# Kernel optimization log

Measured on AMD Instinct MI355X. Metric: run time of the kernel, lower is better.

The kernel has to match this reference:

```python
import jax, jax.numpy as jnp
import numpy as np

D = 1024
H = 16
HD = D // H
MAX_LEN = 5000
LN_EPS = 1e-5


def _pos_encoding(seq_len, d_model, dtype=jnp.float32):
    pos = jnp.arange(seq_len, dtype=jnp.float32)[:, None]                      # [S,1]
    div = jnp.exp(jnp.arange(0, d_model, 2, dtype=jnp.float32) * (-np.log(10000.0) / d_model))
    pe = jnp.zeros((seq_len, d_model), dtype=jnp.float32)
    pe = pe.at[:, 0::2].set(jnp.sin(pos * div))
    pe = pe.at[:, 1::2].set(jnp.cos(pos * div))
    return pe.astype(dtype)                                                    # [S,D]


def _layer_norm(x, g, b):
    mu = jnp.mean(x, axis=-1, keepdims=True)
    var = jnp.mean(jnp.square(x - mu), axis=-1, keepdims=True)
    return (x - mu) * jax.lax.rsqrt(var + LN_EPS) * g + b


def setup_inputs() -> dict:
    key = jax.random.key(0)
    ks = jax.random.split(key, 12)
    B, S = 2, 2048
    s = 1.0 / np.sqrt(D)
    return {
        "key": jax.random.normal(ks[0], (B, S, D), jnp.float32),
        "value": jax.random.normal(ks[1], (B, S, D), jnp.float32),
        "query": jax.random.normal(ks[2], (B, S, D), jnp.float32),
        "Wq": jax.random.normal(ks[3], (D, D), jnp.float32) * s,
        "Wk": jax.random.normal(ks[4], (D, D), jnp.float32) * s,
        "Wv": jax.random.normal(ks[5], (D, D), jnp.float32) * s,
        "Wo": jax.random.normal(ks[6], (D, D), jnp.float32) * s,
        "W1": jax.random.normal(ks[7], (D, D), jnp.float32) * s,
        "b1": jnp.zeros((D,), jnp.float32),
        "W2": jax.random.normal(ks[8], (D, D), jnp.float32) * s,
        "b2": jnp.zeros((D,), jnp.float32),
        "ln1_g": jnp.ones((D,), jnp.float32),
        "ln1_b": jnp.zeros((D,), jnp.float32),
        "ln2_g": jnp.ones((D,), jnp.float32),
        "ln2_b": jnp.zeros((D,), jnp.float32),
    }


def reference(key, value, query, Wq, Wk, Wv, Wo, W1, b1, W2, b2, ln1_g, ln1_b, ln2_g, ln2_b):
    B, S, _ = query.shape
    pe = _pos_encoding(S, D, query.dtype)                 # [S,D]
    k = key + pe
    v = value + pe
    q = query + pe
    # QKV projections (torch Linear: x @ W.T), split heads -> [B,H,S,HD]
    qh = (q @ Wq.T).reshape(B, S, H, HD).transpose(0, 2, 1, 3)
    kh = (k @ Wk.T).reshape(B, S, H, HD).transpose(0, 2, 1, 3)
    vh = (v @ Wv.T).reshape(B, S, H, HD).transpose(0, 2, 1, 3)
    # scaled dot-product attention (full score matrix, as in source)
    scores = jnp.einsum('bhqd,bhkd->bhqk', qh, kh) / np.sqrt(HD)
    attn = jax.nn.softmax(scores, axis=-1)
    ctx = jnp.einsum('bhqk,bhkd->bhqd', attn, vh)         # [B,H,S,HD]
    ctx = ctx.transpose(0, 2, 1, 3).reshape(B, S, D)
    attn_out = ctx @ Wo.T
    # add & norm (residual = pos-encoded query)
    x = _layer_norm(attn_out + q, ln1_g, ln1_b)
    # position-wise FFN (hidden == input_dim)
    ff = jax.nn.relu(x @ W1.T + b1) @ W2.T + b2
    return _layer_norm(ff + x, ln2_g, ln2_b)
```

## Files before the change

kernel.cpp:

```cpp
#include <hip/hip_runtime.h>
#include <hip/hip_bf16.h>
#include <math.h>


#define B_ 2
#define S_ 2048
#define D_ 1024
#define H_ 16
#define HD_ 64

typedef __bf16 bf16_t;
typedef __bf16 bf16x8 __attribute__((ext_vector_type(8)));
typedef __bf16 bf16x4v __attribute__((ext_vector_type(4)));
typedef float f32x4 __attribute__((ext_vector_type(4)));
typedef float f32x16 __attribute__((ext_vector_type(16)));
typedef unsigned int u32;

__device__ __forceinline__ f32x4 mfma16(bf16x8 a, bf16x8 b, f32x4 c) {
  return __builtin_amdgcn_mfma_f32_16x16x32_bf16(a, b, c, 0, 0, 0);
}
__device__ __forceinline__ f32x16 mfma32(bf16x8 a, bf16x8 b, f32x16 c) {
  return __builtin_amdgcn_mfma_f32_32x32x16_bf16(a, b, c, 0, 0, 0);
}
__device__ __forceinline__ u32 pkbf(float a, float b) {
  union { bf16_t h[2]; u32 u; } t;
  t.h[0] = (bf16_t)a; t.h[1] = (bf16_t)b;
  return t.u;
}

__device__ __forceinline__ void gload_lds16(const bf16_t* g, bf16_t* l) {
  __builtin_amdgcn_global_load_lds((const __attribute__((address_space(1))) void*)g,
                                   (__attribute__((address_space(3))) void*)l,
                                   16, 0, 0);
}

__global__ __launch_bounds__(256) void cvtw_kernel(
    const float* __restrict__ w0, const float* __restrict__ w1,
    const float* __restrict__ w2, const float* __restrict__ w3,
    const float* __restrict__ w4, const float* __restrict__ w5,
    bf16_t* __restrict__ dst) {
  const int wsel = blockIdx.y;
  const float* src = wsel == 0 ? w0 : wsel == 1 ? w1 : wsel == 2 ? w2
                   : wsel == 3 ? w3 : wsel == 4 ? w4 : w5;
  const size_t off = (size_t)blockIdx.x * 1024 + threadIdx.x * 4;
  float4 v = *(const float4*)(src + off);
  bf16x4v r;
  r[0] = (bf16_t)v.x; r[1] = (bf16_t)v.y; r[2] = (bf16_t)v.z; r[3] = (bf16_t)v.w;
  *(bf16x4v*)(dst + (size_t)wsel * (D_ * D_) + off) = r;
}

__global__ __launch_bounds__(256) void addpe_kernel(
    const float* __restrict__ q, const float* __restrict__ k,
    const float* __restrict__ v,
    bf16_t* __restrict__ qo, bf16_t* __restrict__ ko, bf16_t* __restrict__ vo) {
  const int row = blockIdx.x;
  const int s = row & (S_ - 1);
  const int d0 = threadIdx.x * 4;
  const size_t base = (size_t)row * D_ + d0;
  float pe[4];
#pragma unroll
  for (int p = 0; p < 2; ++p) {
    float div = __expf((float)(d0 + 2 * p) * -0.008994473019508f);
    float ang = (float)s * div;
    pe[2 * p]     = sinf(ang);
    pe[2 * p + 1] = cosf(ang);
  }
  float4 qv = *(const float4*)&q[base];
  float4 kv = *(const float4*)&k[base];
  float4 vv = *(const float4*)&v[base];
  bf16x4v qr, kr, vr;
  qr[0] = (bf16_t)(qv.x + pe[0]); qr[1] = (bf16_t)(qv.y + pe[1]);
  qr[2] = (bf16_t)(qv.z + pe[2]); qr[3] = (bf16_t)(qv.w + pe[3]);
  kr[0] = (bf16_t)(kv.x + pe[0]); kr[1] = (bf16_t)(kv.y + pe[1]);
  kr[2] = (bf16_t)(kv.z + pe[2]); kr[3] = (bf16_t)(kv.w + pe[3]);
  vr[0] = (bf16_t)(vv.x + pe[0]); vr[1] = (bf16_t)(vv.y + pe[1]);
  vr[2] = (bf16_t)(vv.z + pe[2]); vr[3] = (bf16_t)(vv.w + pe[3]);
  *(bf16x4v*)&qo[base] = qr;
  *(bf16x4v*)&ko[base] = kr;
  *(bf16x4v*)&vo[base] = vr;
}

template <int EPI>
__global__ __launch_bounds__(256) void gemm_s(
    const bf16_t* __restrict__ A, const bf16_t* __restrict__ Wb,
    const float* __restrict__ bias, bf16_t* __restrict__ C) {
  constexpr int Kd = 1024, NT = Kd / 32;
  __shared__ alignas(16) bf16_t As[2][128 * 32];
  __shared__ alignas(16) bf16_t Bs[2][64 * 32];
  const int t = threadIdx.x, lane = t & 63, wid = t >> 6;
  const int m0 = blockIdx.y * 128, n0 = blockIdx.x * 64;

  const bf16_t* Asrc0 = A + (size_t)(m0 + wid * 16 + (lane >> 2)) * Kd + (lane & 3) * 8;
  const bf16_t* Asrc1 = Asrc0 + (size_t)64 * Kd;
  const bf16_t* Wsrc = Wb + (size_t)(n0 + wid * 16 + (lane >> 2)) * Kd + (lane & 3) * 8;

  const f32x4 zero = {0.f, 0.f, 0.f, 0.f};
  f32x4 acc[4][2];
#pragma unroll
  for (int m = 0; m < 4; ++m) { acc[m][0] = zero; acc[m][1] = zero; }

  gload_lds16(Asrc0, &As[0][wid * 512]);
  gload_lds16(Asrc1, &As[0][2048 + wid * 512]);
  gload_lds16(Wsrc,  &Bs[0][wid * 512]);

  const int wr = wid >> 1, wc = wid & 1;
#pragma unroll 2
  for (int kt = 0; kt < NT; ++kt) {
    __syncthreads();
    const int cur = kt & 1, nxt = cur ^ 1;
    if (kt + 1 < NT) {
      const int k0 = (kt + 1) * 32;
      gload_lds16(Asrc0 + k0, &As[nxt][wid * 512]);
      gload_lds16(Asrc1 + k0, &As[nxt][2048 + wid * 512]);
      gload_lds16(Wsrc + k0,  &Bs[nxt][wid * 512]);
    }
    bf16x8 af[4], bfr[2];
#pragma unroll
    for (int m = 0; m < 4; ++m)
      af[m] = *(const bf16x8*)&As[cur][(wr * 64 + m * 16 + (lane & 15)) * 32 + (lane >> 4) * 8];
#pragma unroll
    for (int n = 0; n < 2; ++n)
      bfr[n] = *(const bf16x8*)&Bs[cur][(wc * 32 + n * 16 + (lane & 15)) * 32 + (lane >> 4) * 8];
    __builtin_amdgcn_s_setprio(1);
#pragma unroll
    for (int m = 0; m < 4; ++m)
#pragma unroll
      for (int n = 0; n < 2; ++n)
        acc[m][n] = mfma16(af[m], bfr[n], acc[m][n]);
    __builtin_amdgcn_s_setprio(0);
  }

  const int rbase = m0 + wr * 64 + (lane >> 4) * 4;
  const int cbase = n0 + wc * 32 + (lane & 15);
#pragma unroll
  for (int n = 0; n < 2; ++n) {
    const int col = cbase + n * 16;
    float bv = (EPI >= 1) ? bias[col] : 0.f;
#pragma unroll
    for (int m = 0; m < 4; ++m)
#pragma unroll
      for (int r = 0; r < 4; ++r) {
        float vv = acc[m][n][r] + bv;
        if (EPI == 2) vv = fmaxf(vv, 0.f);
        C[(size_t)(rbase + m * 16 + r) * D_ + col] = (bf16_t)vv;
      }
  }
}

__global__ __launch_bounds__(256) void gemm_qkv(
    const bf16_t* __restrict__ a0p, const bf16_t* __restrict__ a1p,
    const bf16_t* __restrict__ a2p,
    const bf16_t* __restrict__ w0p, const bf16_t* __restrict__ w1p,
    const bf16_t* __restrict__ w2p,
    bf16_t* __restrict__ o0, bf16_t* __restrict__ o1, bf16_t* __restrict__ o2) {
  constexpr int Kd = 1024, NT = Kd / 32;
  __shared__ alignas(16) bf16_t As[2][128 * 32];
  __shared__ alignas(16) bf16_t Bs[2][128 * 32];
  const int t = threadIdx.x, lane = t & 63, wid = t >> 6;
  const int g = lane >> 4, c16 = lane & 15;
  const int m0 = blockIdx.y * 128, n0 = blockIdx.x * 128;

  const bf16_t* A = a0p;
  const bf16_t* Wb = w0p;
  if (blockIdx.z == 1) { A = a1p; Wb = w1p; }
  else if (blockIdx.z == 2) { A = a2p; Wb = w2p; }

  const bf16_t* Asrc0 = A + (size_t)(m0 + wid * 16 + (lane >> 2)) * Kd + (lane & 3) * 8;
  const bf16_t* Asrc1 = Asrc0 + (size_t)64 * Kd;
  const bf16_t* Wsrc0 = Wb + (size_t)(n0 + wid * 16 + (lane >> 2)) * Kd + (lane & 3) * 8;
  const bf16_t* Wsrc1 = Wsrc0 + (size_t)64 * Kd;

  const f32x4 zero = {0.f, 0.f, 0.f, 0.f};
  f32x4 acc[4][4];
#pragma unroll
  for (int m = 0; m < 4; ++m)
#pragma unroll
    for (int n = 0; n < 4; ++n) acc[m][n] = zero;

  gload_lds16(Asrc0, &As[0][wid * 512]);
  gload_lds16(Asrc1, &As[0][2048 + wid * 512]);
  gload_lds16(Wsrc0, &Bs[0][wid * 512]);
  gload_lds16(Wsrc1, &Bs[0][2048 + wid * 512]);

  const int wr = wid >> 1, wc = wid & 1;
#pragma unroll 2
  for (int kt = 0; kt < NT; ++kt) {
    __syncthreads();
    const int cur = kt & 1, nxt = cur ^ 1;
    if (kt + 1 < NT) {
      const int k0 = (kt + 1) * 32;
      gload_lds16(Asrc0 + k0, &As[nxt][wid * 512]);
      gload_lds16(Asrc1 + k0, &As[nxt][2048 + wid * 512]);
      gload_lds16(Wsrc0 + k0, &Bs[nxt][wid * 512]);
      gload_lds16(Wsrc1 + k0, &Bs[nxt][2048 + wid * 512]);
    }
    bf16x8 af[4], bfr[4];
#pragma unroll
    for (int m = 0; m < 4; ++m)
      af[m] = *(const bf16x8*)&As[cur][(wr * 64 + m * 16 + c16) * 32 + g * 8];
#pragma unroll
    for (int n = 0; n < 4; ++n)
      bfr[n] = *(const bf16x8*)&Bs[cur][(wc * 64 + n * 16 + c16) * 32 + g * 8];
    __builtin_amdgcn_s_setprio(1);
#pragma unroll
    for (int m = 0; m < 4; ++m)
#pragma unroll
      for (int n = 0; n < 4; ++n)
        acc[m][n] = mfma16(af[m], bfr[n], acc[m][n]);
    __builtin_amdgcn_s_setprio(0);
  }

  const int rbase = m0 + wr * 64 + g * 4;
  const int cbase = n0 + wc * 64 + c16;
  if (blockIdx.z == 2) {
#pragma unroll
    for (int n = 0; n < 4; ++n) {
      const int col = cbase + n * 16;
#pragma unroll
      for (int m = 0; m < 4; ++m)
#pragma unroll
        for (int r = 0; r < 4; ++r) {
          const int row = rbase + m * 16 + r;
          const int bb = row >> 11, ss = row & (S_ - 1);
          o2[(size_t)bb * D_ * S_ + (size_t)col * S_ + ss] = (bf16_t)acc[m][n][r];
        }
    }
  } else {
    bf16_t* C = (blockIdx.z == 1) ? o1 : o0;
#pragma unroll
    for (int n = 0; n < 4; ++n) {
      const int col = cbase + n * 16;
#pragma unroll
      for (int m = 0; m < 4; ++m)
#pragma unroll
        for (int r = 0; r < 4; ++r)
          C[(size_t)(rbase + m * 16 + r) * D_ + col] = (bf16_t)acc[m][n][r];
    }
  }
}

__global__ __launch_bounds__(256) void attn_kernel(
    const bf16_t* __restrict__ Q, const bf16_t* __restrict__ K,
    const bf16_t* __restrict__ Vt, bf16_t* __restrict__ O) {
  constexpr int NT = S_ / 64;
  constexpr float THR = 11.5416f;
  __shared__ alignas(16) bf16_t Ks[2][64 * 64];
  __shared__ alignas(16) bf16_t Vs[2][64 * 64];
  const int t = threadIdx.x, lane = t & 63, wid = t >> 6;
  const int b = blockIdx.y >> 4, h = blockIdx.y & 15;
  const int qw = blockIdx.x * 128 + wid * 32;
  const int q31 = lane & 31, hi = lane >> 5;

  bf16x8 qb[4];
  {
    const size_t qrow = (size_t)(b * S_ + qw + q31) * D_ + h * HD_ + hi * 8;
#pragma unroll
    for (int ksl = 0; ksl < 4; ++ksl) {
      bf16x8 v = *(const bf16x8*)&Q[qrow + ksl * 16];
#pragma unroll
      for (int j = 0; j < 8; ++j)
        v[j] = (bf16_t)((float)v[j] * (0.125f * 1.44269504f));
      qb[ksl] = v;
    }
  }
  bf16x8 onesb;
#pragma unroll
  for (int j = 0; j < 8; ++j) onesb[j] = (bf16_t)1.0f;

  f32x16 ctx0 = {0.f,0.f,0.f,0.f,0.f,0.f,0.f,0.f,0.f,0.f,0.f,0.f,0.f,0.f,0.f,0.f};
  f32x16 ctx1 = ctx0, lf = ctx0;
  float mrow = -1e30f;

  int sw[4];
#pragma unroll
  for (int x = 0; x < 4; ++x) sw[x] = ((x * 2 + hi) ^ (q31 & 7)) * 8;

  const int trow = wid * 8 + (lane >> 3);
  const int krow_g = (trow & ~12) | ((trow & 4) << 1) | ((trow & 8) >> 1);
  const int lslot = ((lane & 7) ^ ((lane >> 3) & 7)) * 8;
  const bf16_t* Ksrc0 = K + (size_t)(b * S_ + krow_g) * D_ + h * HD_ + lslot;
  const bf16_t* Ksrc1 = K + (size_t)(b * S_ + 32 + krow_g) * D_ + h * HD_ + lslot;
  const bf16_t* Vsrc0 = Vt + (size_t)b * D_ * S_ + (size_t)(h * HD_ + trow) * S_ + lslot;
  const bf16_t* Vsrc1 = Vt + (size_t)b * D_ * S_ + (size_t)(h * HD_ + 32 + trow) * S_ + lslot;

  gload_lds16(Ksrc0, &Ks[0][wid * 512]);
  gload_lds16(Ksrc1, &Ks[0][2048 + wid * 512]);
  gload_lds16(Vsrc0, &Vs[0][wid * 512]);
  gload_lds16(Vsrc1, &Vs[0][2048 + wid * 512]);

#pragma unroll 2
  for (int kt = 0; kt < NT; ++kt) {
    __syncthreads();
    const int cur = kt & 1, nxt = cur ^ 1;
    if (kt + 1 < NT) {
      const size_t ko = (size_t)(kt + 1) * 64 * D_;
      gload_lds16(Ksrc0 + ko, &Ks[nxt][wid * 512]);
      gload_lds16(Ksrc1 + ko, &Ks[nxt][2048 + wid * 512]);
      const size_t vo = (size_t)(kt + 1) * 64;
      gload_lds16(Vsrc0 + vo, &Vs[nxt][wid * 512]);
      gload_lds16(Vsrc1 + vo, &Vs[nxt][2048 + wid * 512]);
    }

    f32x16 s0 = {0.f,0.f,0.f,0.f,0.f,0.f,0.f,0.f,0.f,0.f,0.f,0.f,0.f,0.f,0.f,0.f};
    f32x16 s1 = s0;
    __builtin_amdgcn_s_setprio(1);
#pragma unroll
    for (int ksl = 0; ksl < 4; ++ksl) {
      bf16x8 kb0 = *(const bf16x8*)&Ks[cur][q31 * 64 + sw[ksl]];
      bf16x8 kb1 = *(const bf16x8*)&Ks[cur][(32 + q31) * 64 + sw[ksl]];
      s0 = mfma32(kb0, qb[ksl], s0);
      s1 = mfma32(kb1, qb[ksl], s1);
    }
    __builtin_amdgcn_s_setprio(0);

    float mt = fmaxf(s0[0], s1[0]);
#pragma unroll
    for (int r = 1; r < 16; ++r) mt = fmaxf(mt, fmaxf(s0[r], s1[r]));
    mt = fmaxf(mt, __shfl_xor(mt, 32));
    if (__any(mt > mrow + THR)) {
      float mnew = fmaxf(mrow, mt);
      float scl = exp2f(mrow - mnew);
      mrow = mnew;
#pragma unroll
      for (int r = 0; r < 16; ++r) {
        float sc = __shfl(scl, (r & 3) + 8 * (r >> 2) + 4 * hi);
        ctx0[r] *= sc; ctx1[r] *= sc; lf[r] *= sc;
      }
    }
#pragma unroll
    for (int r = 0; r < 16; ++r) {
      s0[r] = exp2f(s0[r] - mrow);
      s1[r] = exp2f(s1[r] - mrow);
    }

    bf16x8 pa[4];
#pragma unroll
    for (int ks = 0; ks < 4; ++ks) {
      union { u32 w[4]; bf16x8 v; } u;
      if (ks < 2) {
#pragma unroll
        for (int w = 0; w < 4; ++w)
          u.w[w] = pkbf(s0[(ks & 1) * 8 + 2 * w], s0[(ks & 1) * 8 + 2 * w + 1]);
      } else {
#pragma unroll
        for (int w = 0; w < 4; ++w)
          u.w[w] = pkbf(s1[(ks & 1) * 8 + 2 * w], s1[(ks & 1) * 8 + 2 * w + 1]);
      }
      pa[ks] = u.v;
    }

    __builtin_amdgcn_s_setprio(1);
#pragma unroll
    for (int ks = 0; ks < 4; ++ks) lf = mfma32(pa[ks], onesb, lf);
#pragma unroll
    for (int ks = 0; ks < 4; ++ks) {
      bf16x8 vb0 = *(const bf16x8*)&Vs[cur][q31 * 64 + sw[ks]];
      bf16x8 vb1 = *(const bf16x8*)&Vs[cur][(32 + q31) * 64 + sw[ks]];
      ctx0 = mfma32(pa[ks], vb0, ctx0);
      ctx1 = mfma32(pa[ks], vb1, ctx1);
    }
    __builtin_amdgcn_s_setprio(0);
  }

#pragma unroll
  for (int r = 0; r < 16; ++r) {
    const int q = (r & 3) + 8 * (r >> 2) + 4 * hi;
    const float inv = 1.f / lf[r];
    const size_t ro = (size_t)(b * S_ + qw + q) * D_ + h * HD_ + q31;
    O[ro]      = (bf16_t)(ctx0[r] * inv);
    O[ro + 32] = (bf16_t)(ctx1[r] * inv);
  }
}

template <typename OUT>
__global__ __launch_bounds__(256) void add_ln_kernel(
    const bf16_t* __restrict__ a, const bf16_t* __restrict__ res,
    const float* __restrict__ g, const float* __restrict__ be,
    OUT* __restrict__ out) {
  const int t = threadIdx.x;
  const int d0 = t * 4;
  const size_t base = (size_t)blockIdx.x * D_ + d0;
  bf16x4v av = *(const bf16x4v*)&a[base];
  bf16x4v rv = *(const bf16x4v*)&res[base];
  float x[4];
  float s1 = 0.f, s2 = 0.f;
#pragma unroll
  for (int e = 0; e < 4; ++e) {
    x[e] = (float)av[e] + (float)rv[e];
    s1 += x[e];
    s2 += x[e] * x[e];
  }
#pragma unroll
  for (int o = 32; o > 0; o >>= 1) {
    s1 += __shfl_down(s1, o);
    s2 += __shfl_down(s2, o);
  }
  __shared__ float red[8];
  const int lane = t & 63, wid = t >> 6;
  if (lane == 0) { red[wid] = s1; red[4 + wid] = s2; }
  __syncthreads();
  if (t == 0) {
    float t1 = red[0] + red[1] + red[2] + red[3];
    float t2 = red[4] + red[5] + red[6] + red[7];
    float mu = t1 * (1.f / D_);
    float var = t2 * (1.f / D_) - mu * mu;
    red[0] = mu;
    red[1] = rsqrtf(var + 1e-5f);
  }
  __syncthreads();
  const float mu = red[0], rstd = red[1];
  const float4 gv = *(const float4*)&g[d0];
  const float4 bv = *(const float4*)&be[d0];
  float y[4];
  y[0] = (x[0] - mu) * rstd * gv.x + bv.x;
  y[1] = (x[1] - mu) * rstd * gv.y + bv.y;
  y[2] = (x[2] - mu) * rstd * gv.z + bv.z;
  y[3] = (x[3] - mu) * rstd * gv.w + bv.w;
  if constexpr (sizeof(OUT) == 2) {
    bf16x4v o;
    o[0] = (bf16_t)y[0]; o[1] = (bf16_t)y[1]; o[2] = (bf16_t)y[2]; o[3] = (bf16_t)y[3];
    *(bf16x4v*)&out[base] = o;
  } else {
    float4 o = {y[0], y[1], y[2], y[3]};
    *(float4*)&out[base] = o;
  }
}

extern "C" void kernel_launch(void* const* d_in, const int* in_sizes, int n_in,
                              void* d_out, int out_size, void* d_ws, size_t ws_size,
                              hipStream_t stream) {
  const float* key   = (const float*)d_in[0];
  const float* value = (const float*)d_in[1];
  const float* query = (const float*)d_in[2];
  const float* Wq = (const float*)d_in[3];
  const float* Wk = (const float*)d_in[4];
  const float* Wv = (const float*)d_in[5];
  const float* Wo = (const float*)d_in[6];
  const float* W1 = (const float*)d_in[7];
  const float* b1 = (const float*)d_in[8];
  const float* W2 = (const float*)d_in[9];
  const float* b2 = (const float*)d_in[10];
  const float* g1 = (const float*)d_in[11];
  const float* be1 = (const float*)d_in[12];
  const float* g2 = (const float*)d_in[13];
  const float* be2 = (const float*)d_in[14];
  float* out = (float*)d_out;

  bf16_t* ws = (bf16_t*)d_ws;
  const size_t NB = (size_t)B_ * S_ * D_;
  bf16_t* qpe = ws + 0 * NB;
  bf16_t* kpe = ws + 1 * NB;
  bf16_t* vpe = ws + 2 * NB;
  bf16_t* Qp  = ws + 3 * NB;
  bf16_t* Kp  = ws + 4 * NB;
  bf16_t* Vt  = ws + 5 * NB;
  bf16_t* ctx = kpe;
  bf16_t* ao  = vpe;
  bf16_t* x1  = Qp;
  bf16_t* hh  = Kp;
  bf16_t* ff  = Vt;

  bf16_t* wb = (bf16_t*)d_out;
  const size_t WN = (size_t)D_ * D_;
  bf16_t* Wqb = wb + 0 * WN;
  bf16_t* Wkb = wb + 1 * WN;
  bf16_t* Wvb = wb + 2 * WN;
  bf16_t* Wob = wb + 3 * WN;
  bf16_t* W1b = wb + 4 * WN;
  bf16_t* W2b = wb + 5 * WN;

  dim3 sgrid(D_ / 64, (B_ * S_) / 128);

  cvtw_kernel<<<dim3(D_ * D_ / 1024, 6), 256, 0, stream>>>(
      Wq, Wk, Wv, Wo, W1, W2, wb);
  addpe_kernel<<<B_ * S_, 256, 0, stream>>>(query, key, value, qpe, kpe, vpe);

  gemm_qkv<<<dim3(D_ / 128, (B_ * S_) / 128, 3), 256, 0, stream>>>(
      qpe, kpe, vpe, Wqb, Wkb, Wvb, Qp, Kp, Vt);

  attn_kernel<<<dim3(S_ / 128, B_ * H_), 256, 0, stream>>>(Qp, Kp, Vt, ctx);

  gemm_s<0><<<sgrid, 256, 0, stream>>>(ctx, Wob, nullptr, ao);
  add_ln_kernel<bf16_t><<<B_ * S_, 256, 0, stream>>>(ao, qpe, g1, be1, x1);

  gemm_s<2><<<sgrid, 256, 0, stream>>>(x1, W1b, b1, hh);
  gemm_s<1><<<sgrid, 256, 0, stream>>>(hh, W2b, b2, ff);
  add_ln_kernel<float><<<B_ * S_, 256, 0, stream>>>(ff, x1, g2, be2, out);
}
```

Baseline: 223.4 us.

## Split attention over two key halves and merge partial softmax results

Attention now runs as a split-K (flash-decoding style) grid with a z dimension of 2. Each block processes half of the key sequence and writes its normalized partial output along with the per-row max and sum. A new merge kernel combines the two partials using log-sum-exp weights. The aim is to double the number of attention blocks (512 → 1024) so the 256 CUs stay busier. The cost is an extra kernel launch and extra traffic for the partial outputs. The LDS swizzle pattern also changes.

```diff
diff --git a/kernel.cpp b/kernel.cpp
--- a/kernel.cpp
+++ b/kernel.cpp
@@ -241,15 +241,18 @@
 
 __global__ __launch_bounds__(256) void attn_kernel(
     const bf16_t* __restrict__ Q, const bf16_t* __restrict__ K,
-    const bf16_t* __restrict__ Vt, bf16_t* __restrict__ O) {
-  constexpr int NT = S_ / 64;
+    const bf16_t* __restrict__ Vt, bf16_t* __restrict__ O0,
+    bf16_t* __restrict__ O1, float* __restrict__ lm) {
+  constexpr int NT = (S_ / 2) / 64;
   constexpr float THR = 11.5416f;
   __shared__ alignas(16) bf16_t Ks[2][64 * 64];
   __shared__ alignas(16) bf16_t Vs[2][64 * 64];
   const int t = threadIdx.x, lane = t & 63, wid = t >> 6;
   const int b = blockIdx.y >> 4, h = blockIdx.y & 15;
+  const int z = blockIdx.z;
   const int qw = blockIdx.x * 128 + wid * 32;
   const int q31 = lane & 31, hi = lane >> 5;
+  bf16_t* __restrict__ Op = z ? O1 : O0;
 
   bf16x8 qb[4];
   {
@@ -271,17 +274,20 @@
   f32x16 ctx1 = ctx0, lf = ctx0;
   float mrow = -1e30f;
 
+  const int srow5 = (q31 & 7) ^ ((q31 >> 3) & 3);
   int sw[4];
 #pragma unroll
-  for (int x = 0; x < 4; ++x) sw[x] = ((x * 2 + hi) ^ (q31 & 7)) * 8;
+  for (int x = 0; x < 4; ++x) sw[x] = ((x * 2 + hi) ^ srow5) * 8;
 
   const int trow = wid * 8 + (lane >> 3);
   const int krow_g = (trow & ~12) | ((trow & 4) << 1) | ((trow & 8) >> 1);
-  const int lslot = ((lane & 7) ^ ((lane >> 3) & 7)) * 8;
-  const bf16_t* Ksrc0 = K + (size_t)(b * S_ + krow_g) * D_ + h * HD_ + lslot;
-  const bf16_t* Ksrc1 = K + (size_t)(b * S_ + 32 + krow_g) * D_ + h * HD_ + lslot;
-  const bf16_t* Vsrc0 = Vt + (size_t)b * D_ * S_ + (size_t)(h * HD_ + trow) * S_ + lslot;
-  const bf16_t* Vsrc1 = Vt + (size_t)b * D_ * S_ + (size_t)(h * HD_ + 32 + trow) * S_ + lslot;
+  const int st5 = (trow & 7) ^ ((trow >> 3) & 3);
+  const int lslot = ((lane & 7) ^ st5) * 8;
+  const size_t zoff = (size_t)z * (S_ / 2);
+  const bf16_t* Ksrc0 = K + (size_t)(b * S_ + zoff + krow_g) * D_ + h * HD_ + lslot;
+  const bf16_t* Ksrc1 = K + (size_t)(b * S_ + zoff + 32 + krow_g) * D_ + h * HD_ + lslot;
+  const bf16_t* Vsrc0 = Vt + (size_t)b * D_ * S_ + (size_t)(h * HD_ + trow) * S_ + zoff + lslot;
+  const bf16_t* Vsrc1 = Vt + (size_t)b * D_ * S_ + (size_t)(h * HD_ + 32 + trow) * S_ + zoff + lslot;
 
   gload_lds16(Ksrc0, &Ks[0][wid * 512]);
   gload_lds16(Ksrc1, &Ks[0][2048 + wid * 512]);
@@ -362,14 +368,48 @@
     __builtin_amdgcn_s_setprio(0);
   }
 
+  const size_t lmbase = ((size_t)(z * B_ + b) * H_ + h) * S_ + qw;
+  constexpr size_t LOFF = (size_t)2 * B_ * H_ * S_;
 #pragma unroll
   for (int r = 0; r < 16; ++r) {
     const int q = (r & 3) + 8 * (r >> 2) + 4 * hi;
+    const float mq = __shfl(mrow, q);
     const float inv = 1.f / lf[r];
     const size_t ro = (size_t)(b * S_ + qw + q) * D_ + h * HD_ + q31;
-    O[ro]      = (bf16_t)(ctx0[r] * inv);
-    O[ro + 32] = (bf16_t)(ctx1[r] * inv);
-  }
+    Op[ro]      = (bf16_t)(ctx0[r] * inv);
+    Op[ro + 32] = (bf16_t)(ctx1[r] * inv);
+    if (q31 == 0) {
+      lm[lmbase + q]        = mq;
+      lm[LOFF + lmbase + q] = lf[r];
+    }
+  }
+}
+
+__global__ __launch_bounds__(256) void merge_kernel(
+    const bf16_t* __restrict__ O0, const bf16_t* __restrict__ O1,
+    const float* __restrict__ lm, bf16_t* __restrict__ ctx) {
+  const int row = blockIdx.x;
+  const int b = row >> 11, s = row & (S_ - 1);
+  const int d0 = threadIdx.x * 4;
+  const int h = d0 >> 6;
+  const size_t base = (size_t)row * D_ + d0;
+  constexpr size_t LOFF = (size_t)2 * B_ * H_ * S_;
+  const size_t i0 = ((size_t)b * H_ + h) * S_ + s;
+  const size_t i1 = ((size_t)(B_ + b) * H_ + h) * S_ + s;
+  const float m0 = lm[i0], m1 = lm[i1];
+  const float l0 = lm[LOFF + i0], l1 = lm[LOFF + i1];
+  const float M = fmaxf(m0, m1);
+  float w0 = exp2f(m0 - M) * l0;
+  float w1 = exp2f(m1 - M) * l1;
+  const float inv = 1.f / (w0 + w1);
+  w0 *= inv; w1 *= inv;
+  bf16x4v a = *(const bf16x4v*)&O0[base];
+  bf16x4v c = *(const bf16x4v*)&O1[base];
+  bf16x4v o;
+#pragma unroll
+  for (int e = 0; e < 4; ++e)
+    o[e] = (bf16_t)(w0 * (float)a[e] + w1 * (float)c[e]);
+  *(bf16x4v*)&ctx[base] = o;
 }
 
 template <typename OUT>
@@ -454,6 +494,8 @@
   bf16_t* Qp  = ws + 3 * NB;
   bf16_t* Kp  = ws + 4 * NB;
   bf16_t* Vt  = ws + 5 * NB;
+  bf16_t* Op0 = kpe;
+  bf16_t* Op1 = vpe;
   bf16_t* ctx = kpe;
   bf16_t* ao  = vpe;
   bf16_t* x1  = Qp;
@@ -468,6 +510,7 @@
   bf16_t* Wob = wb + 3 * WN;
   bf16_t* W1b = wb + 4 * WN;
   bf16_t* W2b = wb + 5 * WN;
+  float* lm = (float*)d_out + 3 * 1024 * 1024;
 
   dim3 sgrid(D_ / 64, (B_ * S_) / 128);
 
@@ -478,7 +521,9 @@
   gemm_qkv<<<dim3(D_ / 128, (B_ * S_) / 128, 3), 256, 0, stream>>>(
       qpe, kpe, vpe, Wqb, Wkb, Wvb, Qp, Kp, Vt);
 
-  attn_kernel<<<dim3(S_ / 128, B_ * H_), 256, 0, stream>>>(Qp, Kp, Vt, ctx);
+  attn_kernel<<<dim3(S_ / 128, B_ * H_, 2), 256, 0, stream>>>(
+      Qp, Kp, Vt, Op0, Op1, lm);
+  merge_kernel<<<B_ * S_, 256, 0, stream>>>(Op0, Op1, lm, ctx);
 
   gemm_s<0><<<sgrid, 256, 0, stream>>>(ctx, Wob, nullptr, ao);
   add_ln_kernel<bf16_t><<<B_ * S_, 256, 0, stream>>>(ao, qpe, g1, be1, x1);
```

Measured after the change: 234.0 us. 4.8% more time.
